# Performance work log

Measured on AMD Instinct MI355X. Metric: run time of the kernel, lower is better.

Reference implementation:

```python
import jax, jax.numpy as jnp
import numpy as np

N = 100000      # num nodes
E = 1600000     # num edges (no self-loops; forward appends N self-loops)
DIN = 256       # in_channels
H = 1           # heads
C = 64          # out_channels per head
NEG = 0.2       # leaky_relu negative slope
NID = N // 10   # number of ID nodes


def setup_inputs() -> dict:
    key = jax.random.key(0)
    ks = jax.random.split(key, 7)
    x = jax.random.normal(ks[0], (N, DIN), jnp.float32)
    src = jax.random.randint(ks[1], (E,), 0, N, dtype=jnp.int32)
    off = jax.random.randint(ks[2], (E,), 1, N, dtype=jnp.int32)
    dst = ((src.astype(jnp.int64) + off.astype(jnp.int64)) % N).astype(jnp.int32)  # guarantees no self-loops
    edge_index = jnp.stack([src, dst])  # [2, E], row0 = source j, row1 = target i
    node_id = jax.random.randint(ks[3], (NID,), 0, N, dtype=jnp.int32)
    g = float(1.0 / np.sqrt(DIN))  # glorot-ish scale
    W = jax.random.uniform(ks[4], (DIN, H * C), jnp.float32, -g, g)
    W_id = jax.random.uniform(ks[5], (DIN, H * C), jnp.float32, -g, g)
    att = jax.random.uniform(ks[6], (1, H, 2 * C), jnp.float32, -g, g)
    return dict(x=x, edge_index=edge_index, node_id=node_id, W=W, W_id=W_id, att=att)


def _gat_id_forward(x, W, W_id, att, edge_index, node_id):
    # ID-aware transform: x @ W, plus extra W_id contribution added at id nodes
    x_id = x[node_id] @ W_id                      # [NID, H*C]
    h = x @ W                                     # [N, H*C]
    h = h.at[node_id].add(x_id)
    # add self-loops (inputs contain none)
    loops = jnp.arange(N, dtype=edge_index.dtype)
    src = jnp.concatenate([edge_index[0], loops])  # source j
    dst = jnp.concatenate([edge_index[1], loops])  # target i
    hr = h.reshape(N, H, C)
    xi = hr[dst]                                   # [Et, H, C]
    xj = hr[src]                                   # [Et, H, C]
    # alpha = (cat(x_i, x_j) * att).sum(-1)
    alpha = (xi * att[:, :, :C]).sum(-1) + (xj * att[:, :, C:]).sum(-1)  # [Et, H]
    alpha = jax.nn.leaky_relu(alpha, NEG)
    # segment softmax over target node (every node has a self-loop -> no empty segments)
    m = jax.ops.segment_max(alpha, dst, num_segments=N)
    alpha = jnp.exp(alpha - m[dst])
    s = jax.ops.segment_sum(alpha, dst, num_segments=N)
    alpha = alpha / (s[dst] + 1e-16)
    # dropout p=0 / eval mode -> no-op
    out = jax.ops.segment_sum(xj * alpha[:, :, None], dst, num_segments=N)  # [N, H, C]
    return out.reshape(N, H * C)  # concat=True, bias=False


def reference(x, edge_index, node_id, W, W_id, att):
    return _gat_id_forward(x, W, W_id, att, edge_index, node_id)
```

## Files before the change

### kernel.cpp

```cpp
#include <hip/hip_runtime.h>
#include <hip/hip_bf16.h>

#define N_NODES 100000
#define E_EDGES 1600000
#define DIN 256
#define C_OUT 64
#define NID_CNT 10000
#define NEG 0.2f
#define NBUCK 391
#define CAP 4608
#define GEMM_BLOCKS 391
#define BIN_BLOCKS 121
#define BIN_EPB 13224
#define BIN_ITERS 26

typedef short bf16x8 __attribute__((ext_vector_type(8)));
typedef float f32x4  __attribute__((ext_vector_type(4)));

__device__ __forceinline__ float lrelu(float x) { return x > 0.f ? x : NEG * x; }
__device__ __forceinline__ unsigned short f2bs(float f) {
    __hip_bfloat16 b = __float2bfloat16(f);
    return *reinterpret_cast<unsigned short*>(&b);
}
__device__ __forceinline__ bf16x8 pack8(float4 a, float4 b) {
    bf16x8 r;
    r[0] = (short)f2bs(a.x); r[1] = (short)f2bs(a.y);
    r[2] = (short)f2bs(a.z); r[3] = (short)f2bs(a.w);
    r[4] = (short)f2bs(b.x); r[5] = (short)f2bs(b.y);
    r[6] = (short)f2bs(b.z); r[7] = (short)f2bs(b.w);
    return r;
}
__device__ __forceinline__ float2 unpk2(unsigned u) {
    return make_float2(__uint_as_float(u << 16), __uint_as_float(u & 0xffff0000u));
}

__global__ __launch_bounds__(256) void k_zero(float* __restrict__ cnt,
                                              int* __restrict__ bkcur) {
    const int t = blockIdx.x * 256 + threadIdx.x;
    if (t < N_NODES) cnt[t] = 0.f;
    if (t < NBUCK) bkcur[t] = t * CAP;
}

__global__ __launch_bounds__(256) void k_prep(const float* __restrict__ W,
                                              const float* __restrict__ Wid,
                                              unsigned short* __restrict__ WtG,
                                              unsigned short* __restrict__ WidtG,
                                              const int* __restrict__ nid,
                                              float* __restrict__ cnt) {
    const int b = blockIdx.x;
    const int tid = threadIdx.x;
    if (b < 128) {
        const int t = b * 256 + tid;
        const int mat = t >> 14;
        const int r = t & 16383;
        const int k = r >> 6, c = r & 63;
        if (mat == 0) WtG[c * DIN + k] = f2bs(W[(long)k * C_OUT + c]);
        else          WidtG[c * DIN + k] = f2bs(Wid[(long)k * C_OUT + c]);
    } else {
        const int t = (b - 128) * 256 + tid;
        if (t < NID_CNT) atomicAdd(&cnt[nid[t]], 1.0f);
    }
}

__global__ __launch_bounds__(512, 4) void k_mega(const float* __restrict__ x,
                                                 const unsigned short* __restrict__ WtG,
                                                 const unsigned short* __restrict__ WidtG,
                                                 const float* __restrict__ cnt,
                                                 const float* __restrict__ att,
                                                 __hip_bfloat16* __restrict__ hb,
                                                 float* __restrict__ ad,
                                                 float* __restrict__ as,
                                                 const int* __restrict__ ei,
                                                 int* __restrict__ bkcur,
                                                 unsigned* __restrict__ binned) {
    __shared__ __align__(16) char smem[66560];
    const int blk = blockIdx.x;
    const int tid = threadIdx.x;

    if (blk < GEMM_BLOCKS) {
        char* wlds = smem;
        float* cnt_lds = (float*)(smem + 65536);
        const int w = tid >> 6, l = tid & 63;
        const int g = l >> 4, cl = l & 15;
        const int r0 = blk * 256;

        #pragma unroll
        for (int i = 0; i < 4; ++i) {
            int f = tid + i * 512;
            int c = f >> 5, s = f & 31;
            int byte = c * 512 + ((s ^ (c & 7)) << 4);
            *(bf16x8*)(wlds + byte)         = *(const bf16x8*)(WtG + (long)c * DIN + s * 8);
            *(bf16x8*)(wlds + 32768 + byte) = *(const bf16x8*)(WidtG + (long)c * DIN + s * 8);
        }
        if (tid < 256) cnt_lds[tid] = (r0 + tid < N_NODES) ? cnt[r0 + tid] : 0.f;
        __syncthreads();

        f32x4 acc1[2][4] = {};
        f32x4 acc2[2][4] = {};

        const int row0 = r0 + w * 32 + cl;
        const float* xp0 = x + (long)min(row0, N_NODES - 1) * DIN + g * 8;
        const float* xp1 = x + (long)min(row0 + 16, N_NODES - 1) * DIN + g * 8;

        float4 xb[2][4];
        xb[0][0] = *(const float4*)(xp0);
        xb[0][1] = *(const float4*)(xp0 + 4);
        xb[0][2] = *(const float4*)(xp1);
        xb[0][3] = *(const float4*)(xp1 + 4);
        #pragma unroll
        for (int kt = 0; kt < 8; ++kt) {
            if (kt < 7) {
                const int nb = (kt + 1) & 1;
                xb[nb][0] = *(const float4*)(xp0 + (kt + 1) * 32);
                xb[nb][1] = *(const float4*)(xp0 + (kt + 1) * 32 + 4);
                xb[nb][2] = *(const float4*)(xp1 + (kt + 1) * 32);
                xb[nb][3] = *(const float4*)(xp1 + (kt + 1) * 32 + 4);
            }
            const int cb = kt & 1;
            bf16x8 a0 = pack8(xb[cb][0], xb[cb][1]);
            bf16x8 a1 = pack8(xb[cb][2], xb[cb][3]);
            #pragma unroll
            for (int ct = 0; ct < 4; ++ct) {
                int c = ct * 16 + cl;
                int byte = c * 512 + (((kt * 4 + g) ^ (c & 7)) << 4);
                bf16x8 bw = *(const bf16x8*)(wlds + byte);
                bf16x8 bi = *(const bf16x8*)(wlds + 32768 + byte);
                acc1[0][ct] = __builtin_amdgcn_mfma_f32_16x16x32_bf16(a0, bw, acc1[0][ct], 0, 0, 0);
                acc1[1][ct] = __builtin_amdgcn_mfma_f32_16x16x32_bf16(a1, bw, acc1[1][ct], 0, 0, 0);
                acc2[0][ct] = __builtin_amdgcn_mfma_f32_16x16x32_bf16(a0, bi, acc2[0][ct], 0, 0, 0);
                acc2[1][ct] = __builtin_amdgcn_mfma_f32_16x16x32_bf16(a1, bi, acc2[1][ct], 0, 0, 0);
            }
        }
        __syncthreads();

        float attv1[4], attv2[4];
        #pragma unroll
        for (int ct = 0; ct < 4; ++ct) {
            attv1[ct] = att[ct * 16 + cl];
            attv2[ct] = att[C_OUT + ct * 16 + cl];
        }
        unsigned short* hbt = (unsigned short*)wlds;
        #pragma unroll
        for (int rt = 0; rt < 2; ++rt) {
            #pragma unroll
            for (int reg = 0; reg < 4; ++reg) {
                const int rbl = w * 32 + rt * 16 + g * 4 + reg;
                const float cv = cnt_lds[rbl];
                float pd = 0.f, ps = 0.f;
                #pragma unroll
                for (int ct = 0; ct < 4; ++ct) {
                    float hv = acc1[rt][ct][reg] + cv * acc2[rt][ct][reg];
                    pd += hv * attv1[ct];
                    ps += hv * attv2[ct];
                    hbt[rbl * 72 + ct * 16 + cl] = f2bs(hv);
                }
                #pragma unroll
                for (int o = 1; o < 16; o <<= 1) {
                    pd += __shfl_xor(pd, o, 64);
                    ps += __shfl_xor(ps, o, 64);
                }
                if (cl == 0) {
                    int grow = r0 + rbl;
                    if (grow < N_NODES) { ad[grow] = pd; as[grow] = ps; }
                }
            }
        }
        __syncthreads();
        #pragma unroll
        for (int i = 0; i < 4; ++i) {
            int f = tid + i * 512;
            int row = f >> 3, s = f & 7;
            int grow = r0 + row;
            if (grow < N_NODES) {
                bf16x8 v = *(const bf16x8*)(wlds + row * 144 + s * 16);
                *(bf16x8*)((unsigned short*)hb + (long)grow * C_OUT + s * 8) = v;
            }
        }
    } else {
        int* cnt_s = (int*)smem;
        int* base  = cnt_s + NBUCK;
        int* lcur  = base + NBUCK;
        const int b2 = blk - GEMM_BLOCKS;
        const int e0 = b2 * BIN_EPB;
        const int e1 = min(e0 + BIN_EPB, E_EDGES);
        for (int i = tid; i < NBUCK; i += 512) cnt_s[i] = 0;
        __syncthreads();
        int se[BIN_ITERS], de[BIN_ITERS];
        #pragma unroll
        for (int j = 0; j < BIN_ITERS; ++j) {
            int e = e0 + j * 512 + tid;
            if (e < e1) {
                se[j] = ei[e];
                de[j] = ei[E_EDGES + e];
                atomicAdd(&cnt_s[de[j] >> 8], 1);
            } else de[j] = -1;
        }
        __syncthreads();
        for (int i = tid; i < NBUCK; i += 512) {
            base[i] = cnt_s[i] ? atomicAdd(&bkcur[i], cnt_s[i]) : 0;
            lcur[i] = 0;
        }
        __syncthreads();
        #pragma unroll
        for (int j = 0; j < BIN_ITERS; ++j) {
            if (de[j] >= 0) {
                int bb = de[j] >> 8;
                int r = atomicAdd(&lcur[bb], 1);
                binned[base[bb] + r] = ((unsigned)se[j] << 8) | (unsigned)(de[j] & 255);
            }
        }
    }
}

__global__ __launch_bounds__(256) void k_place(const unsigned* __restrict__ binned,
                                               const int* __restrict__ bkcur,
                                               int* __restrict__ csr,
                                               int* __restrict__ cur) {
    __shared__ int ncnt[256];
    __shared__ int tmp[256];
    __shared__ int ncur[256];
    const int tid = threadIdx.x;
    const int b = blockIdx.x;
    const int lo = b * CAP;
    const int n = bkcur[b] - lo;
    const int node0 = b << 8;
    ncnt[tid] = 0;
    __syncthreads();
    for (int e = tid; e < n; e += 256)
        atomicAdd(&ncnt[binned[lo + e] & 255u], 1);
    __syncthreads();
    const int v = ncnt[tid];
    tmp[tid] = v;
    __syncthreads();
    for (int o = 1; o < 256; o <<= 1) {
        int t = (tid >= o) ? tmp[tid - o] : 0;
        __syncthreads();
        tmp[tid] += t;
        __syncthreads();
    }
    const int incl = tmp[tid];
    if (node0 + tid < N_NODES) cur[node0 + tid] = lo + incl;
    ncur[tid] = incl - v;
    __syncthreads();
    for (int e = tid; e < n; e += 256) {
        unsigned p = binned[lo + e];
        int r = atomicAdd(&ncur[p & 255u], 1);
        csr[lo + r] = (int)(p >> 8);
    }
}

__global__ __launch_bounds__(256) void k_gather(const int* __restrict__ cur,
                                                const int* __restrict__ csr,
                                                const unsigned* __restrict__ hb2,
                                                const float* __restrict__ ad,
                                                const float* __restrict__ as,
                                                float* __restrict__ out) {
    const int lane = threadIdx.x & 63;
    const int lg = lane & 31;
    const int gb = lane & 32;
    const int i = blockIdx.x * 8 + ((threadIdx.x >> 6) << 1) + (lane >> 5);
    if (i >= N_NODES) return;
    const int end   = cur[i];
    const int start = (i & 255) ? cur[i - 1] : (i >> 8) * CAP;
    const int deg   = end - start;
    const float adi = ad[i];
    const float asi = as[i];
    float2 acc;
    float den;
    if (deg <= 32) {
        int s = 0; float a = -1e30f;
        if (lg < deg) { s = csr[start + lg]; a = as[s]; }
        float mx = fmaxf(a, asi);
        #pragma unroll
        for (int o = 16; o > 0; o >>= 1) mx = fmaxf(mx, __shfl_xor(mx, o, 64));
        const float m = lrelu(adi + mx);
        float w = (lg < deg) ? __expf(lrelu(adi + a) - m) : 0.f;
        const float wself = __expf(lrelu(adi + asi) - m);
        float wsum = w;
        #pragma unroll
        for (int o = 16; o > 0; o >>= 1) wsum += __shfl_xor(wsum, o, 64);
        den = wself + wsum;
        float2 hv = unpk2(hb2[(long)i * 32 + lg]);
        acc = make_float2(wself * hv.x, wself * hv.y);
        int j = 0;
        for (; j + 4 <= deg; j += 4) {
            int   s0 = __shfl(s, gb + j, 64),     s1 = __shfl(s, gb + j + 1, 64),
                  s2 = __shfl(s, gb + j + 2, 64), s3 = __shfl(s, gb + j + 3, 64);
            float w0 = __shfl(w, gb + j, 64),     w1 = __shfl(w, gb + j + 1, 64),
                  w2 = __shfl(w, gb + j + 2, 64), w3 = __shfl(w, gb + j + 3, 64);
            float2 h0 = unpk2(hb2[(long)s0 * 32 + lg]);
            float2 h1 = unpk2(hb2[(long)s1 * 32 + lg]);
            float2 h2 = unpk2(hb2[(long)s2 * 32 + lg]);
            float2 h3 = unpk2(hb2[(long)s3 * 32 + lg]);
            acc.x += w0 * h0.x; acc.y += w0 * h0.y;
            acc.x += w1 * h1.x; acc.y += w1 * h1.y;
            acc.x += w2 * h2.x; acc.y += w2 * h2.y;
            acc.x += w3 * h3.x; acc.y += w3 * h3.y;
        }
        for (; j < deg; ++j) {
            int   sj = __shfl(s, gb + j, 64);
            float wj = __shfl(w, gb + j, 64);
            float2 hj = unpk2(hb2[(long)sj * 32 + lg]);
            acc.x += wj * hj.x; acc.y += wj * hj.y;
        }
    } else {
        float mx = asi;
        for (int b = 0; b < deg; b += 32) {
            int idx = b + lg;
            if (idx < deg) mx = fmaxf(mx, as[csr[start + idx]]);
        }
        #pragma unroll
        for (int o = 16; o > 0; o >>= 1) mx = fmaxf(mx, __shfl_xor(mx, o, 64));
        const float m = lrelu(adi + mx);
        const float wself = __expf(lrelu(adi + asi) - m);
        float2 hv = unpk2(hb2[(long)i * 32 + lg]);
        acc = make_float2(wself * hv.x, wself * hv.y);
        den = wself;
        for (int b = 0; b < deg; b += 32) {
            int idx = b + lg;
            int s = 0; float w = 0.f;
            if (idx < deg) {
                s = csr[start + idx];
                w = __expf(lrelu(adi + as[s]) - m);
            }
            const int cnt2 = min(32, deg - b);
            for (int j = 0; j < cnt2; ++j) {
                int   sj = __shfl(s, gb + j, 64);
                float wj = __shfl(w, gb + j, 64);
                float2 hj = unpk2(hb2[(long)sj * 32 + lg]);
                acc.x += wj * hj.x; acc.y += wj * hj.y;
            }
            float wsum = w;
            #pragma unroll
            for (int o = 16; o > 0; o >>= 1) wsum += __shfl_xor(wsum, o, 64);
            den += wsum;
        }
    }
    const float r = 1.f / (den + 1e-16f);
    *(float2*)(out + (long)i * C_OUT + lg * 2) = make_float2(acc.x * r, acc.y * r);
}

extern "C" void kernel_launch(void* const* d_in, const int* in_sizes, int n_in,
                              void* d_out, int out_size, void* d_ws, size_t ws_size,
                              hipStream_t stream) {
    const float* x   = (const float*)d_in[0];
    const int*   ei  = (const int*)d_in[1];
    const int*   nid = (const int*)d_in[2];
    const float* W   = (const float*)d_in[3];
    const float* Wid = (const float*)d_in[4];
    const float* att = (const float*)d_in[5];
    float* out = (float*)d_out;

    char* ws = (char*)d_ws;
    __hip_bfloat16* hb = (__hip_bfloat16*)(ws);
    float* ad    = (float*)(ws + 12800000);
    float* as    = (float*)(ws + 13200000);
    float* cnt   = (float*)(ws + 13600000);
    int*   cur   = (int*)  (ws + 14000000);
    unsigned* binned = (unsigned*)(ws + 14400000);
    int*   csr   = (int*)  (ws + 21700000);
    unsigned short* WtG  = (unsigned short*)(ws + 29000000);
    unsigned short* WidG = (unsigned short*)(ws + 29032768);
    int*   bkcur = (int*)  (ws + 29065536);

    k_zero<<<393, 256, 0, stream>>>(cnt, bkcur);
    k_prep<<<168, 256, 0, stream>>>(W, Wid, WtG, WidG, nid, cnt);
    k_mega<<<512, 512, 0, stream>>>(x, WtG, WidG, cnt, att, hb, ad, as, ei, bkcur, binned);
    k_place<<<NBUCK, 256, 0, stream>>>(binned, bkcur, csr, cur);
    k_gather<<<12500, 256, 0, stream>>>(cur, csr, (const unsigned*)hb, ad, as, out);
}
```

Measured before the change: 109.4 us.

## Stage x tiles through LDS as bf16 with coalesced loads, halving rows per block

The GEMM part of the mega kernel now loads x with fully coalesced row-contiguous float4 reads, converts them to bf16 and stores them into a swizzled LDS buffer. The MFMA A-fragments are then read from LDS in two K-halves, with the second half's global load overlapped with the first half's compute. Block row count drops from 256 to 128, which doubles the GEMM block count, and LDS grows to about 128KB per block. This aims to fix the strided per-lane global access pattern on x, at the cost of lower occupancy (launch bounds reduced to 2 blocks) and extra LDS traffic and syncs.

```diff
diff --git a/kernel.cpp b/kernel.cpp
--- a/kernel.cpp
+++ b/kernel.cpp
@@ -9,7 +9,7 @@
 #define NEG 0.2f
 #define NBUCK 391
 #define CAP 4608
-#define GEMM_BLOCKS 391
+#define GEMM_BLOCKS 782
 #define BIN_BLOCKS 121
 #define BIN_EPB 13224
 #define BIN_ITERS 26
@@ -22,12 +22,10 @@
     __hip_bfloat16 b = __float2bfloat16(f);
     return *reinterpret_cast<unsigned short*>(&b);
 }
-__device__ __forceinline__ bf16x8 pack8(float4 a, float4 b) {
-    bf16x8 r;
-    r[0] = (short)f2bs(a.x); r[1] = (short)f2bs(a.y);
-    r[2] = (short)f2bs(a.z); r[3] = (short)f2bs(a.w);
-    r[4] = (short)f2bs(b.x); r[5] = (short)f2bs(b.y);
-    r[6] = (short)f2bs(b.z); r[7] = (short)f2bs(b.w);
+__device__ __forceinline__ uint2 pack4(float4 v) {
+    uint2 r;
+    r.x = ((unsigned)f2bs(v.y) << 16) | f2bs(v.x);
+    r.y = ((unsigned)f2bs(v.w) << 16) | f2bs(v.z);
     return r;
 }
 __device__ __forceinline__ float2 unpk2(unsigned u) {
@@ -62,7 +60,7 @@
     }
 }
 
-__global__ __launch_bounds__(512, 4) void k_mega(const float* __restrict__ x,
+__global__ __launch_bounds__(512, 2) void k_mega(const float* __restrict__ x,
                                                  const unsigned short* __restrict__ WtG,
                                                  const unsigned short* __restrict__ WidtG,
                                                  const float* __restrict__ cnt,
@@ -73,17 +71,26 @@
                                                  const int* __restrict__ ei,
                                                  int* __restrict__ bkcur,
                                                  unsigned* __restrict__ binned) {
-    __shared__ __align__(16) char smem[66560];
+    __shared__ __align__(16) char smem[131584];
     const int blk = blockIdx.x;
     const int tid = threadIdx.x;
 
     if (blk < GEMM_BLOCKS) {
         char* wlds = smem;
-        float* cnt_lds = (float*)(smem + 65536);
+        char* xh   = smem + 65536;
+        float* cnt_lds = (float*)(smem + 131072);
         const int w = tid >> 6, l = tid & 63;
         const int g = l >> 4, cl = l & 15;
-        const int r0 = blk * 256;
-
+        const int l31 = l & 31, rh = l >> 5;
+        const int r0 = blk * 128;
+
+        float4 xv[8];
+        #pragma unroll
+        for (int j = 0; j < 8; ++j) {
+            int row = w * 16 + j * 2 + rh;
+            int grow = min(r0 + row, N_NODES - 1);
+            xv[j] = *(const float4*)(x + (long)grow * DIN + l31 * 4);
+        }
         #pragma unroll
         for (int i = 0; i < 4; ++i) {
             int f = tid + i * 512;
@@ -92,43 +99,58 @@
             *(bf16x8*)(wlds + byte)         = *(const bf16x8*)(WtG + (long)c * DIN + s * 8);
             *(bf16x8*)(wlds + 32768 + byte) = *(const bf16x8*)(WidtG + (long)c * DIN + s * 8);
         }
-        if (tid < 256) cnt_lds[tid] = (r0 + tid < N_NODES) ? cnt[r0 + tid] : 0.f;
-        __syncthreads();
-
-        f32x4 acc1[2][4] = {};
-        f32x4 acc2[2][4] = {};
-
-        const int row0 = r0 + w * 32 + cl;
-        const float* xp0 = x + (long)min(row0, N_NODES - 1) * DIN + g * 8;
-        const float* xp1 = x + (long)min(row0 + 16, N_NODES - 1) * DIN + g * 8;
-
-        float4 xb[2][4];
-        xb[0][0] = *(const float4*)(xp0);
-        xb[0][1] = *(const float4*)(xp0 + 4);
-        xb[0][2] = *(const float4*)(xp1);
-        xb[0][3] = *(const float4*)(xp1 + 4);
-        #pragma unroll
-        for (int kt = 0; kt < 8; ++kt) {
-            if (kt < 7) {
-                const int nb = (kt + 1) & 1;
-                xb[nb][0] = *(const float4*)(xp0 + (kt + 1) * 32);
-                xb[nb][1] = *(const float4*)(xp0 + (kt + 1) * 32 + 4);
-                xb[nb][2] = *(const float4*)(xp1 + (kt + 1) * 32);
-                xb[nb][3] = *(const float4*)(xp1 + (kt + 1) * 32 + 4);
-            }
-            const int cb = kt & 1;
-            bf16x8 a0 = pack8(xb[cb][0], xb[cb][1]);
-            bf16x8 a1 = pack8(xb[cb][2], xb[cb][3]);
+        if (tid < 128) cnt_lds[tid] = (r0 + tid < N_NODES) ? cnt[r0 + tid] : 0.f;
+        #pragma unroll
+        for (int j = 0; j < 8; ++j) {
+            int row = w * 16 + j * 2 + rh;
+            int byte = row * 256 + (((l31 >> 1) ^ (row & 15)) << 4) + (l31 & 1) * 8;
+            *(uint2*)(xh + byte) = pack4(xv[j]);
+        }
+        #pragma unroll
+        for (int j = 0; j < 8; ++j) {
+            int row = w * 16 + j * 2 + rh;
+            int grow = min(r0 + row, N_NODES - 1);
+            xv[j] = *(const float4*)(x + (long)grow * DIN + 128 + l31 * 4);
+        }
+        __syncthreads();
+
+        f32x4 acc1[4] = {};
+        f32x4 acc2[4] = {};
+        const int arow = w * 16 + cl;
+        const int axor = (arow & 15);
+
+        #pragma unroll
+        for (int kt = 0; kt < 4; ++kt) {
+            bf16x8 a0 = *(const bf16x8*)(xh + arow * 256 + (((kt * 4 + g) ^ axor) << 4));
             #pragma unroll
             for (int ct = 0; ct < 4; ++ct) {
                 int c = ct * 16 + cl;
-                int byte = c * 512 + (((kt * 4 + g) ^ (c & 7)) << 4);
-                bf16x8 bw = *(const bf16x8*)(wlds + byte);
-                bf16x8 bi = *(const bf16x8*)(wlds + 32768 + byte);
-                acc1[0][ct] = __builtin_amdgcn_mfma_f32_16x16x32_bf16(a0, bw, acc1[0][ct], 0, 0, 0);
-                acc1[1][ct] = __builtin_amdgcn_mfma_f32_16x16x32_bf16(a1, bw, acc1[1][ct], 0, 0, 0);
-                acc2[0][ct] = __builtin_amdgcn_mfma_f32_16x16x32_bf16(a0, bi, acc2[0][ct], 0, 0, 0);
-                acc2[1][ct] = __builtin_amdgcn_mfma_f32_16x16x32_bf16(a1, bi, acc2[1][ct], 0, 0, 0);
+                int wbyte = c * 512 + (((kt * 4 + g) ^ (c & 7)) << 4);
+                bf16x8 bw = *(const bf16x8*)(wlds + wbyte);
+                bf16x8 bi = *(const bf16x8*)(wlds + 32768 + wbyte);
+                acc1[ct] = __builtin_amdgcn_mfma_f32_16x16x32_bf16(a0, bw, acc1[ct], 0, 0, 0);
+                acc2[ct] = __builtin_amdgcn_mfma_f32_16x16x32_bf16(a0, bi, acc2[ct], 0, 0, 0);
+            }
+        }
+        #pragma unroll
+        for (int j = 0; j < 8; ++j) {
+            int row = w * 16 + j * 2 + rh;
+            int byte = 32768 + row * 256 + (((l31 >> 1) ^ (row & 15)) << 4) + (l31 & 1) * 8;
+            *(uint2*)(xh + byte) = pack4(xv[j]);
+        }
+        __syncthreads();
+        #pragma unroll
+        for (int kt = 4; kt < 8; ++kt) {
+            int kt2 = kt - 4;
+            bf16x8 a0 = *(const bf16x8*)(xh + 32768 + arow * 256 + (((kt2 * 4 + g) ^ axor) << 4));
+            #pragma unroll
+            for (int ct = 0; ct < 4; ++ct) {
+                int c = ct * 16 + cl;
+                int wbyte = c * 512 + (((kt * 4 + g) ^ (c & 7)) << 4);
+                bf16x8 bw = *(const bf16x8*)(wlds + wbyte);
+                bf16x8 bi = *(const bf16x8*)(wlds + 32768 + wbyte);
+                acc1[ct] = __builtin_amdgcn_mfma_f32_16x16x32_bf16(a0, bw, acc1[ct], 0, 0, 0);
+                acc2[ct] = __builtin_amdgcn_mfma_f32_16x16x32_bf16(a0, bi, acc2[ct], 0, 0, 0);
             }
         }
         __syncthreads();
@@ -141,33 +163,30 @@
         }
         unsigned short* hbt = (unsigned short*)wlds;
         #pragma unroll
-        for (int rt = 0; rt < 2; ++rt) {
-            #pragma unroll
-            for (int reg = 0; reg < 4; ++reg) {
-                const int rbl = w * 32 + rt * 16 + g * 4 + reg;
-                const float cv = cnt_lds[rbl];
-                float pd = 0.f, ps = 0.f;
-                #pragma unroll
-                for (int ct = 0; ct < 4; ++ct) {
-                    float hv = acc1[rt][ct][reg] + cv * acc2[rt][ct][reg];
-                    pd += hv * attv1[ct];
-                    ps += hv * attv2[ct];
-                    hbt[rbl * 72 + ct * 16 + cl] = f2bs(hv);
-                }
-                #pragma unroll
-                for (int o = 1; o < 16; o <<= 1) {
-                    pd += __shfl_xor(pd, o, 64);
-                    ps += __shfl_xor(ps, o, 64);
-                }
-                if (cl == 0) {
-                    int grow = r0 + rbl;
-                    if (grow < N_NODES) { ad[grow] = pd; as[grow] = ps; }
-                }
-            }
-        }
-        __syncthreads();
-        #pragma unroll
-        for (int i = 0; i < 4; ++i) {
+        for (int reg = 0; reg < 4; ++reg) {
+            const int rbl = w * 16 + g * 4 + reg;
+            const float cv = cnt_lds[rbl];
+            float pd = 0.f, ps = 0.f;
+            #pragma unroll
+            for (int ct = 0; ct < 4; ++ct) {
+                float hv = acc1[ct][reg] + cv * acc2[ct][reg];
+                pd += hv * attv1[ct];
+                ps += hv * attv2[ct];
+                hbt[rbl * 72 + ct * 16 + cl] = f2bs(hv);
+            }
+            #pragma unroll
+            for (int o = 1; o < 16; o <<= 1) {
+                pd += __shfl_xor(pd, o, 64);
+                ps += __shfl_xor(ps, o, 64);
+            }
+            if (cl == 0) {
+                int grow = r0 + rbl;
+                if (grow < N_NODES) { ad[grow] = pd; as[grow] = ps; }
+            }
+        }
+        __syncthreads();
+        #pragma unroll
+        for (int i = 0; i < 2; ++i) {
             int f = tid + i * 512;
             int row = f >> 3, s = f & 7;
             int grow = r0 + row;
@@ -365,7 +384,8 @@
 
     k_zero<<<393, 256, 0, stream>>>(cnt, bkcur);
     k_prep<<<168, 256, 0, stream>>>(W, Wid, WtG, WidG, nid, cnt);
-    k_mega<<<512, 512, 0, stream>>>(x, WtG, WidG, cnt, att, hb, ad, as, ei, bkcur, binned);
+    k_mega<<<GEMM_BLOCKS + BIN_BLOCKS, 512, 0, stream>>>(x, WtG, WidG, cnt, att,
+                                                         hb, ad, as, ei, bkcur, binned);
     k_place<<<NBUCK, 256, 0, stream>>>(binned, bkcur, csr, cur);
     k_gather<<<12500, 256, 0, stream>>>(cur, csr, (const unsigned*)hb, ad, as, out);
 }
```

New measurement: 121.1 us. +10.7%, slower.
